# Performance work log

Measured on AMD Instinct MI355X. Metric: run time of the kernel, lower is better.

## Reference

```python
import jax, jax.numpy as jnp
import numpy as np

N, D, H, O = 2048, 128, 256, 1  # batch, input_dim, hidden_dim, output_dim
LN_EPS = 1e-5


def setup_inputs() -> dict:
    key = jax.random.key(0)
    ks = jax.random.split(key, 10)
    s = lambda fan_in: 1.0 / np.sqrt(fan_in)
    return {
        "array": jax.random.normal(ks[0], (N, D), dtype=jnp.float32),
        # per-feature Linear(1, H) stacked: weight [D, H], bias [D, H]
        "W_in": jax.random.uniform(ks[1], (D, H), jnp.float32, -1.0, 1.0),
        "b_in": jax.random.uniform(ks[2], (D, H), jnp.float32, -1.0, 1.0),
        # FactorAttentionLayer (width D): W: Linear(D, D), V: Linear(D, 1), LayerNorm(D)
        "Wf": jax.random.uniform(ks[3], (D, D), jnp.float32, -s(D), s(D)),
        "bf": jax.random.uniform(ks[4], (D,), jnp.float32, -s(D), s(D)),
        "Vf": jax.random.uniform(ks[5], (D,), jnp.float32, -s(D), s(D)),
        "bv": jnp.zeros((), jnp.float32),
        "ln_g": jnp.ones((D,), jnp.float32),
        "ln_b": jnp.zeros((D,), jnp.float32),
        # fc_hidden: Linear(D*H, H); fc_output: Linear(H, O)  (stored as [in, out])
        "Wh": jax.random.uniform(ks[6], (D * H, H), jnp.float32, -s(D * H), s(D * H)),
        "bh": jax.random.uniform(ks[7], (H,), jnp.float32, -s(D * H), s(D * H)),
        "Wo": jax.random.uniform(ks[8], (H, O), jnp.float32, -s(H), s(H)),
        "bo": jax.random.uniform(ks[9], (O,), jnp.float32, -s(H), s(H)),
    }


def reference(array, W_in, b_in, Wf, bf, Vf, bv, ln_g, ln_b, Wh, bh, Wo, bo):
    # Fused per-feature Linear(1,H)+ReLU: [n, D, H]
    p = jax.nn.relu(array[:, :, None] * W_in[None] + b_in[None])
    # permute(0, 2, 1) -> [n, H, D]
    x = jnp.transpose(p, (0, 2, 1))
    # FactorAttention: tanh-linear, softmax over axis 1 (the H axis), residual mul, LayerNorm over D
    u = jnp.tanh(jnp.einsum('nhd,de->nhe', x, Wf) + bf)          # [n, H, D]
    scores = jnp.einsum('nhd,d->nh', u, Vf) + bv                  # [n, H]
    attn = jax.nn.softmax(scores, axis=1)[:, :, None]             # [n, H, 1]
    y = x + x * attn                                              # [n, H, D]
    mu = jnp.mean(y, axis=-1, keepdims=True)
    var = jnp.mean((y - mu) ** 2, axis=-1, keepdims=True)
    y = (y - mu) * jax.lax.rsqrt(var + LN_EPS) * ln_g + ln_b
    # flatten [n, H*D] and MLP head (dropout = identity in eval)
    xx = y.reshape(y.shape[0], -1)
    h = jax.nn.relu(xx @ Wh + bh)
    return h @ Wo + bo
```

## Files before the change

kernel.cpp:

```cpp
#include <hip/hip_runtime.h>

#define NB 2048
#define DD 128
#define HH 256
#define KF 32768
#define LN_EPS 1e-5f

typedef __attribute__((ext_vector_type(8))) short short8;
typedef __attribute__((ext_vector_type(4))) float float4_t;

__device__ __forceinline__ unsigned short f2bf(float f) {
    unsigned int u = __builtin_bit_cast(unsigned int, f);
    u += 0x7fffu + ((u >> 16) & 1u);
    return (unsigned short)(u >> 16);
}

__device__ __forceinline__ void gl2lds16(const void* g, void* l) {
    __builtin_amdgcn_global_load_lds(
        (const __attribute__((address_space(1))) unsigned int*)g,
        (__attribute__((address_space(3))) unsigned int*)l, 16, 0, 0);
}

__global__ void prep_b(const float* __restrict__ Wh, unsigned short* __restrict__ WhbT) {
    __shared__ unsigned short tile[64][65];
    int kb = blockIdx.x;
    int jb = blockIdx.y;
    int t = threadIdx.x;
    int c = t & 63, r4 = t >> 6;
    int kap0 = kb * 64;
    int d  = kap0 >> 8;
    int h0 = kap0 & 255;
    for (int rr = r4; rr < 64; rr += 4) {
        int k = (h0 + rr) * 128 + d;
        tile[rr][c] = f2bf(Wh[(long)k * 256 + jb * 64 + c]);
    }
    __syncthreads();
    for (int rr = r4; rr < 64; rr += 4) {
        WhbT[(long)(jb * 64 + rr) * KF + kap0 + c] = tile[c][rr];
    }
}

__global__ void zgen(const float* __restrict__ arr, const float* __restrict__ Win,
                     const float* __restrict__ bin, const float* __restrict__ g,
                     const float* __restrict__ beta, unsigned short* __restrict__ Z) {
    __shared__ float a_s[4][128];
    __shared__ float g_s[128], b_s[128];
    int t = threadIdx.x;
    int n0 = blockIdx.x * 4;
    if (t < 128) { g_s[t] = g[t]; b_s[t] = beta[t]; }
    for (int i = t; i < 512; i += 256) a_s[i >> 7][i & 127] = arr[n0 * 128 + i];
    __syncthreads();
    int h = t;
    float sum[4] = {0.f, 0.f, 0.f, 0.f}, ssq[4] = {0.f, 0.f, 0.f, 0.f};
    for (int d = 0; d < 128; ++d) {
        float w = Win[d * 256 + h];
        float bb = bin[d * 256 + h];
#pragma unroll
        for (int q = 0; q < 4; ++q) {
            float x = fmaxf(fmaf(a_s[q][d], w, bb), 0.f);
            sum[q] += x; ssq[q] += x * x;
        }
    }
    float mu[4], rs[4];
#pragma unroll
    for (int q = 0; q < 4; ++q) {
        mu[q] = sum[q] * (1.f / 128.f);
        float var = fmaxf(ssq[q] * (1.f / 128.f) - mu[q] * mu[q], 0.f);
        rs[q] = rsqrtf(var + LN_EPS);
    }
    for (int d = 0; d < 128; ++d) {
        float w = Win[d * 256 + h];
        float bb = bin[d * 256 + h];
        float gg = g_s[d], be = b_s[d];
#pragma unroll
        for (int q = 0; q < 4; ++q) {
            float x = fmaxf(fmaf(a_s[q][d], w, bb), 0.f);
            float zv = fmaf((x - mu[q]) * rs[q], gg, be);
            Z[(long)(n0 + q) * KF + d * 256 + h] = f2bf(zv);
        }
    }
}

#define BM 128
#define BN 128
#define BK 32
#define KSPLIT 16
#define KSL (KF / KSPLIT)

__global__ __launch_bounds__(256, 2) void gemm_k(
        const unsigned short* __restrict__ A,
        const unsigned short* __restrict__ Bt,
        float* __restrict__ Cp) {
    __shared__ unsigned short As[BM * BK];
    __shared__ unsigned short Bs[BN * BK];
    int bid = blockIdx.x;
    int ks = bid >> 5;
    int mt = (bid >> 1) & 15;
    int nt = bid & 1;
    int m0 = mt * BM, n0 = nt * BN, k0 = ks * KSL;
    int t = threadIdx.x;
    int lane = t & 63, wave = t >> 6;
    int wm = (wave >> 1) * 64, wn = (wave & 1) * 64;
    int fr = lane & 15;
    int fk = (lane >> 4) * 8;

    float4_t acc[4][4] = {};

    const unsigned short* Aab = A + (long)m0 * KF + k0;
    const unsigned short* Bab = Bt + (long)n0 * KF + k0;
    int s0 = t, s1 = t + 256;
    long aoff0 = (long)(s0 >> 2) * KF + (long)(s0 & 3) * 8;
    long aoff1 = (long)(s1 >> 2) * KF + (long)(s1 & 3) * 8;

    for (int kk = 0; kk < KSL; kk += BK) {
        __syncthreads();
        gl2lds16(Aab + kk + aoff0, &As[s0 * 8]);
        gl2lds16(Aab + kk + aoff1, &As[s1 * 8]);
        gl2lds16(Bab + kk + aoff0, &Bs[s0 * 8]);
        gl2lds16(Bab + kk + aoff1, &Bs[s1 * 8]);
        __syncthreads();
        short8 af[4], bfv[4];
#pragma unroll
        for (int i = 0; i < 4; ++i)
            af[i] = *(const short8*)&As[(wm + i * 16 + fr) * BK + fk];
#pragma unroll
        for (int i = 0; i < 4; ++i)
            bfv[i] = *(const short8*)&Bs[(wn + i * 16 + fr) * BK + fk];
#pragma unroll
        for (int mi = 0; mi < 4; ++mi)
#pragma unroll
            for (int ni = 0; ni < 4; ++ni)
                acc[mi][ni] = __builtin_amdgcn_mfma_f32_16x16x32_bf16(
                    af[mi], bfv[ni], acc[mi][ni], 0, 0, 0);
    }

    int rb = (lane >> 4) * 4;
    float* Cb = Cp + (long)ks * NB * 256;
#pragma unroll
    for (int mi = 0; mi < 4; ++mi) {
#pragma unroll
        for (int ni = 0; ni < 4; ++ni) {
            int n = n0 + wn + ni * 16 + fr;
#pragma unroll
            for (int r = 0; r < 4; ++r) {
                int m = m0 + wm + mi * 16 + rb + r;
                Cb[(long)m * 256 + n] = acc[mi][ni][r];
            }
        }
    }
}

__global__ void finale(const float* __restrict__ Cp, const float* __restrict__ bh,
                       const float* __restrict__ Wo, const float* __restrict__ bo,
                       float* __restrict__ out) {
    __shared__ float red[4];
    int n = blockIdx.x, t = threadIdx.x;
    int lane = t & 63, wave = t >> 6;
    float s = bh[t];
    for (int sl = 0; sl < KSPLIT; ++sl)
        s += Cp[(long)sl * NB * 256 + (long)n * 256 + t];
    float v = fmaxf(s, 0.f) * Wo[t];
#pragma unroll
    for (int o = 32; o; o >>= 1) v += __shfl_down(v, o);
    if (lane == 0) red[wave] = v;
    __syncthreads();
    if (t == 0) out[n] = red[0] + red[1] + red[2] + red[3] + bo[0];
}

extern "C" void kernel_launch(void* const* d_in, const int* in_sizes, int n_in,
                              void* d_out, int out_size, void* d_ws, size_t ws_size,
                              hipStream_t stream) {
    const float* arr  = (const float*)d_in[0];
    const float* Win  = (const float*)d_in[1];
    const float* bin  = (const float*)d_in[2];
    const float* ln_g = (const float*)d_in[7];
    const float* ln_b = (const float*)d_in[8];
    const float* Wh   = (const float*)d_in[9];
    const float* bh   = (const float*)d_in[10];
    const float* Wo   = (const float*)d_in[11];
    const float* bo   = (const float*)d_in[12];
    float* out = (float*)d_out;

    char* ws = (char*)d_ws;
    unsigned short* WhbT = (unsigned short*)ws;
    unsigned short* Z    = (unsigned short*)(ws + 16777216ull);
    float* Cp            = (float*)(ws + 16777216ull + 134217728ull);

    hipLaunchKernelGGL(prep_b, dim3(512, 4), dim3(256), 0, stream, Wh, WhbT);
    hipLaunchKernelGGL(zgen, dim3(512), dim3(256), 0, stream, arr, Win, bin, ln_g, ln_b, Z);
    hipLaunchKernelGGL(gemm_k, dim3(512), dim3(256), 0, stream, Z, WhbT, Cp);
    hipLaunchKernelGGL(finale, dim3(NB), dim3(256), 0, stream, Cp, bh, Wo, bo, out);
}
```

Before: 207.5 us.

## Generate LayerNorm activations inside GEMM and fold gamma/beta into weights

Removes the materialized 128MB bf16 Z activation matrix. The GEMM now recomputes relu(a*W+b) normalized by precomputed per-row mean/rstd on the fly in registers. LayerNorm gamma is folded into the transposed bf16 weight, and beta becomes a precomputed bias vector built with atomics. The GEMM tiling changes to BN=256 with a 32-way K split and an XOR-swizzled B layout in LDS. This trades a large memory write and read for extra ALU work in the GEMM, plus doubled partial-sum traffic in the finale.

After: 210.9 us. Within noise of the previous version (+1.6%).

```diff
diff --git a/kernel.cpp b/kernel.cpp
--- a/kernel.cpp
+++ b/kernel.cpp
@@ -1,146 +1,195 @@
 #include <hip/hip_runtime.h>
 
 #define NB 2048
-#define DD 128
-#define HH 256
 #define KF 32768
 #define LN_EPS 1e-5f
+#define KSPLIT 32
+#define KSL 1024
+#define BM 128
+#define BN 256
+#define BK 32
 
 typedef __attribute__((ext_vector_type(8))) short short8;
 typedef __attribute__((ext_vector_type(4))) float float4_t;
+typedef __attribute__((ext_vector_type(4))) float vf4;
 
 __device__ __forceinline__ unsigned short f2bf(float f) {
     unsigned int u = __builtin_bit_cast(unsigned int, f);
     u += 0x7fffu + ((u >> 16) & 1u);
     return (unsigned short)(u >> 16);
 }
-
+__device__ __forceinline__ unsigned int pk2(float lo, float hi) {
+    return (unsigned int)f2bf(lo) | ((unsigned int)f2bf(hi) << 16);
+}
 __device__ __forceinline__ void gl2lds16(const void* g, void* l) {
     __builtin_amdgcn_global_load_lds(
         (const __attribute__((address_space(1))) unsigned int*)g,
         (__attribute__((address_space(3))) unsigned int*)l, 16, 0, 0);
 }
 
-__global__ void prep_b(const float* __restrict__ Wh, unsigned short* __restrict__ WhbT) {
+__global__ void prep_b(const float* __restrict__ Wh, const float* __restrict__ g,
+                       const float* __restrict__ beta,
+                       unsigned short* __restrict__ GwT, float* __restrict__ Cbeta) {
     __shared__ unsigned short tile[64][65];
-    int kb = blockIdx.x;
-    int jb = blockIdx.y;
-    int t = threadIdx.x;
-    int c = t & 63, r4 = t >> 6;
+    __shared__ float cred[4][64];
+    int kb = blockIdx.x, jb = blockIdx.y;
+    int t = threadIdx.x, c = t & 63, r4 = t >> 6;
     int kap0 = kb * 64;
-    int d  = kap0 >> 8;
-    int h0 = kap0 & 255;
+    int s = kb >> 4, h_loc = kb & 15;
+    int h = (s >> 1) * 16 + h_loc;
+    int dbase = (s & 1) * 64;
+    float cb = 0.f;
     for (int rr = r4; rr < 64; rr += 4) {
-        int k = (h0 + rr) * 128 + d;
-        tile[rr][c] = f2bf(Wh[(long)k * 256 + jb * 64 + c]);
-    }
-    __syncthreads();
+        int d = dbase + rr;
+        float w = Wh[(long)(h * 128 + d) * 256 + jb * 64 + c];
+        tile[rr][c] = f2bf(g[d] * w);
+        cb += beta[d] * w;
+    }
+    cred[r4][c] = cb;
+    __syncthreads();
+    if (r4 == 0)
+        atomicAdd(&Cbeta[jb * 64 + c], cred[0][c] + cred[1][c] + cred[2][c] + cred[3][c]);
     for (int rr = r4; rr < 64; rr += 4) {
-        WhbT[(long)(jb * 64 + rr) * KF + kap0 + c] = tile[c][rr];
-    }
-}
-
-__global__ void zgen(const float* __restrict__ arr, const float* __restrict__ Win,
-                     const float* __restrict__ bin, const float* __restrict__ g,
-                     const float* __restrict__ beta, unsigned short* __restrict__ Z) {
+        int jrow = jb * 64 + rr;
+        int c2 = c & 31;
+        int pos = ((c2 >> 3) ^ ((jrow >> 1) & 3)) & 3;
+        GwT[(long)jrow * KF + kap0 + (c & 32) + pos * 8 + (c & 7)] = tile[c][rr];
+    }
+}
+
+__global__ void trans_wb(const float* __restrict__ Win, const float* __restrict__ bin,
+                         float* __restrict__ WinT, float* __restrict__ binT) {
+    __shared__ float tile[64][65];
+    const float* src = blockIdx.z ? bin : Win;
+    float* dst = blockIdx.z ? binT : WinT;
+    int db = blockIdx.x, hb = blockIdx.y;
+    int t = threadIdx.x, c = t & 63, r4 = t >> 6;
+    for (int rr = r4; rr < 64; rr += 4)
+        tile[rr][c] = src[(db * 64 + rr) * 256 + hb * 64 + c];
+    __syncthreads();
+    for (int rr = r4; rr < 64; rr += 4)
+        dst[(hb * 64 + rr) * 128 + db * 64 + c] = tile[c][rr];
+}
+
+__global__ void stats(const float* __restrict__ arr, const float* __restrict__ Win,
+                      const float* __restrict__ bin, float* __restrict__ rsm) {
     __shared__ float a_s[4][128];
-    __shared__ float g_s[128], b_s[128];
     int t = threadIdx.x;
     int n0 = blockIdx.x * 4;
-    if (t < 128) { g_s[t] = g[t]; b_s[t] = beta[t]; }
     for (int i = t; i < 512; i += 256) a_s[i >> 7][i & 127] = arr[n0 * 128 + i];
     __syncthreads();
-    int h = t;
-    float sum[4] = {0.f, 0.f, 0.f, 0.f}, ssq[4] = {0.f, 0.f, 0.f, 0.f};
+    float sum[4] = {}, ssq[4] = {};
     for (int d = 0; d < 128; ++d) {
-        float w = Win[d * 256 + h];
-        float bb = bin[d * 256 + h];
+        float w = Win[d * 256 + t], bb = bin[d * 256 + t];
 #pragma unroll
         for (int q = 0; q < 4; ++q) {
             float x = fmaxf(fmaf(a_s[q][d], w, bb), 0.f);
             sum[q] += x; ssq[q] += x * x;
         }
     }
-    float mu[4], rs[4];
+    float2* rsm2 = (float2*)rsm;
 #pragma unroll
     for (int q = 0; q < 4; ++q) {
-        mu[q] = sum[q] * (1.f / 128.f);
-        float var = fmaxf(ssq[q] * (1.f / 128.f) - mu[q] * mu[q], 0.f);
-        rs[q] = rsqrtf(var + LN_EPS);
-    }
-    for (int d = 0; d < 128; ++d) {
-        float w = Win[d * 256 + h];
-        float bb = bin[d * 256 + h];
-        float gg = g_s[d], be = b_s[d];
-#pragma unroll
-        for (int q = 0; q < 4; ++q) {
-            float x = fmaxf(fmaf(a_s[q][d], w, bb), 0.f);
-            float zv = fmaf((x - mu[q]) * rs[q], gg, be);
-            Z[(long)(n0 + q) * KF + d * 256 + h] = f2bf(zv);
-        }
-    }
-}
-
-#define BM 128
-#define BN 128
-#define BK 32
-#define KSPLIT 16
-#define KSL (KF / KSPLIT)
-
-__global__ __launch_bounds__(256, 2) void gemm_k(
-        const unsigned short* __restrict__ A,
-        const unsigned short* __restrict__ Bt,
-        float* __restrict__ Cp) {
-    __shared__ unsigned short As[BM * BK];
+        float mu = sum[q] * (1.f / 128.f);
+        float var = fmaxf(ssq[q] * (1.f / 128.f) - mu * mu, 0.f);
+        float rs = rsqrtf(var + LN_EPS);
+        rsm2[(long)(n0 + q) * 256 + t] = make_float2(rs, -mu * rs);
+    }
+}
+
+__global__ __launch_bounds__(256, 2) void gemm_f(
+        const float* __restrict__ arr, const float* __restrict__ WinT,
+        const float* __restrict__ binT, const float* __restrict__ rsm,
+        const unsigned short* __restrict__ GwT, float* __restrict__ Cp) {
+    __shared__ float wi_s[16 * 64];
+    __shared__ float bi_s[16 * 64];
+    __shared__ float rs_s[128 * 17 * 2];
     __shared__ unsigned short Bs[BN * BK];
+
     int bid = blockIdx.x;
-    int ks = bid >> 5;
-    int mt = (bid >> 1) & 15;
-    int nt = bid & 1;
-    int m0 = mt * BM, n0 = nt * BN, k0 = ks * KSL;
-    int t = threadIdx.x;
-    int lane = t & 63, wave = t >> 6;
-    int wm = (wave >> 1) * 64, wn = (wave & 1) * 64;
-    int fr = lane & 15;
-    int fk = (lane >> 4) * 8;
-
-    float4_t acc[4][4] = {};
-
-    const unsigned short* Aab = A + (long)m0 * KF + k0;
-    const unsigned short* Bab = Bt + (long)n0 * KF + k0;
-    int s0 = t, s1 = t + 256;
-    long aoff0 = (long)(s0 >> 2) * KF + (long)(s0 & 3) * 8;
-    long aoff1 = (long)(s1 >> 2) * KF + (long)(s1 & 3) * 8;
-
-    for (int kk = 0; kk < KSL; kk += BK) {
-        __syncthreads();
-        gl2lds16(Aab + kk + aoff0, &As[s0 * 8]);
-        gl2lds16(Aab + kk + aoff1, &As[s1 * 8]);
-        gl2lds16(Bab + kk + aoff0, &Bs[s0 * 8]);
-        gl2lds16(Bab + kk + aoff1, &Bs[s1 * 8]);
-        __syncthreads();
-        short8 af[4], bfv[4];
-#pragma unroll
-        for (int i = 0; i < 4; ++i)
-            af[i] = *(const short8*)&As[(wm + i * 16 + fr) * BK + fk];
-#pragma unroll
-        for (int i = 0; i < 4; ++i)
-            bfv[i] = *(const short8*)&Bs[(wn + i * 16 + fr) * BK + fk];
-#pragma unroll
-        for (int mi = 0; mi < 4; ++mi)
-#pragma unroll
-            for (int ni = 0; ni < 4; ++ni)
-                acc[mi][ni] = __builtin_amdgcn_mfma_f32_16x16x32_bf16(
-                    af[mi], bfv[ni], acc[mi][ni], 0, 0, 0);
-    }
-
-    int rb = (lane >> 4) * 4;
-    float* Cb = Cp + (long)ks * NB * 256;
+    int mt = bid >> 5;
+    int s = bid & 31;
+    int m0 = mt * BM;
+    int hs0 = (s >> 1) * 16;
+    int ds = s & 1;
+    int t = threadIdx.x, lane = t & 63, wave = t >> 6;
+    int fr = lane & 15, kg = lane >> 4;
+    int wm = (wave & 1) * 64, wn = (wave >> 1) * 128;
+
+    gl2lds16(WinT + (hs0 + (t >> 4)) * 128 + ds * 64 + (t & 15) * 4, &wi_s[t * 4]);
+    gl2lds16(binT + (hs0 + (t >> 4)) * 128 + ds * 64 + (t & 15) * 4, &bi_s[t * 4]);
+    const float2* rsm2 = (const float2*)rsm;
+#pragma unroll
+    for (int i = 0; i < 8; ++i) {
+        int ci = t + i * 256;
+        int m = ci >> 4, hl = ci & 15;
+        float2 rv = rsm2[(long)(m0 + m) * 256 + hs0 + hl];
+        *(float2*)&rs_s[(m * 17 + hl) * 2] = rv;
+    }
+
+    float4_t acc[4][8] = {};
+    const unsigned short* Bg = GwT + (long)s * KSL;
+
+    for (int dh = 0; dh < 2; ++dh) {
+        vf4 a0[4], a1[4];
+#pragma unroll
+        for (int mi = 0; mi < 4; ++mi) {
+            const float* ap = arr + (long)(m0 + wm + mi * 16 + fr) * 128
+                              + ds * 64 + dh * 32 + kg * 8;
+            a0[mi] = *(const vf4*)ap;
+            a1[mi] = *(const vf4*)(ap + 4);
+        }
+        for (int hl = 0; hl < 16; ++hl) {
+            int w = hl * 2 + dh;
+            __syncthreads();
+#pragma unroll
+            for (int i = 0; i < 4; ++i) {
+                int ci = t + i * 256;
+                gl2lds16(Bg + (long)(ci >> 2) * KF + w * 32 + (ci & 3) * 8,
+                         &Bs[ci * 8]);
+            }
+            vf4 w0 = *(const vf4*)&wi_s[hl * 64 + dh * 32 + kg * 8];
+            vf4 w1 = *(const vf4*)&wi_s[hl * 64 + dh * 32 + kg * 8 + 4];
+            vf4 b0 = *(const vf4*)&bi_s[hl * 64 + dh * 32 + kg * 8];
+            vf4 b1 = *(const vf4*)&bi_s[hl * 64 + dh * 32 + kg * 8 + 4];
+            short8 af[4];
+#pragma unroll
+            for (int mi = 0; mi < 4; ++mi) {
+                float2 rv = *(const float2*)&rs_s[((wm + mi * 16 + fr) * 17 + hl) * 2];
+                float z[8];
+#pragma unroll
+                for (int j = 0; j < 4; ++j) {
+                    float x = fmaxf(fmaf(a0[mi][j], w0[j], b0[j]), 0.f);
+                    z[j] = fmaf(x, rv.x, rv.y);
+                    float x2 = fmaxf(fmaf(a1[mi][j], w1[j], b1[j]), 0.f);
+                    z[4 + j] = fmaf(x2, rv.x, rv.y);
+                }
+                union { short8 v; unsigned int u[4]; } pa;
+#pragma unroll
+                for (int p = 0; p < 4; ++p) pa.u[p] = pk2(z[2 * p], z[2 * p + 1]);
+                af[mi] = pa.v;
+            }
+            __syncthreads();
+#pragma unroll
+            for (int ni = 0; ni < 8; ++ni) {
+                int n = wn + ni * 16 + fr;
+                int bc = kg ^ ((n >> 1) & 3);
+                short8 bf = *(const short8*)&Bs[n * 32 + bc * 8];
+#pragma unroll
+                for (int mi = 0; mi < 4; ++mi)
+                    acc[mi][ni] = __builtin_amdgcn_mfma_f32_16x16x32_bf16(
+                        af[mi], bf, acc[mi][ni], 0, 0, 0);
+            }
+        }
+    }
+
+    float* Cb = Cp + (long)s * NB * 256;
+    int rb = kg * 4;
 #pragma unroll
     for (int mi = 0; mi < 4; ++mi) {
 #pragma unroll
-        for (int ni = 0; ni < 4; ++ni) {
-            int n = n0 + wn + ni * 16 + fr;
+        for (int ni = 0; ni < 8; ++ni) {
+            int n = wn + ni * 16 + fr;
 #pragma unroll
             for (int r = 0; r < 4; ++r) {
                 int m = m0 + wm + mi * 16 + rb + r;
@@ -150,16 +199,16 @@
     }
 }
 
-__global__ void finale(const float* __restrict__ Cp, const float* __restrict__ bh,
-                       const float* __restrict__ Wo, const float* __restrict__ bo,
-                       float* __restrict__ out) {
+__global__ void finale(const float* __restrict__ Cp, const float* __restrict__ Cbeta,
+                       const float* __restrict__ bh, const float* __restrict__ Wo,
+                       const float* __restrict__ bo, float* __restrict__ out) {
     __shared__ float red[4];
     int n = blockIdx.x, t = threadIdx.x;
     int lane = t & 63, wave = t >> 6;
-    float s = bh[t];
+    float ssum = bh[t] + Cbeta[t];
     for (int sl = 0; sl < KSPLIT; ++sl)
-        s += Cp[(long)sl * NB * 256 + (long)n * 256 + t];
-    float v = fmaxf(s, 0.f) * Wo[t];
+        ssum += Cp[(long)sl * NB * 256 + (long)n * 256 + t];
+    float v = fmaxf(ssum, 0.f) * Wo[t];
 #pragma unroll
     for (int o = 32; o; o >>= 1) v += __shfl_down(v, o);
     if (lane == 0) red[wave] = v;
@@ -182,12 +231,17 @@
     float* out = (float*)d_out;
 
     char* ws = (char*)d_ws;
-    unsigned short* WhbT = (unsigned short*)ws;
-    unsigned short* Z    = (unsigned short*)(ws + 16777216ull);
-    float* Cp            = (float*)(ws + 16777216ull + 134217728ull);
-
-    hipLaunchKernelGGL(prep_b, dim3(512, 4), dim3(256), 0, stream, Wh, WhbT);
-    hipLaunchKernelGGL(zgen, dim3(512), dim3(256), 0, stream, arr, Win, bin, ln_g, ln_b, Z);
-    hipLaunchKernelGGL(gemm_k, dim3(512), dim3(256), 0, stream, Z, WhbT, Cp);
-    hipLaunchKernelGGL(finale, dim3(NB), dim3(256), 0, stream, Cp, bh, Wo, bo, out);
-}
+    unsigned short* GwT  = (unsigned short*)(ws);
+    float*          Cp   = (float*)(ws + 16777216ull);
+    float*          rsm  = (float*)(ws + 83886080ull);
+    float*          WinT = (float*)(ws + 88080384ull);
+    float*          binT = (float*)(ws + 88211456ull);
+    float*          Cbeta= (float*)(ws + 88342528ull);
+
+    hipMemsetAsync(Cbeta, 0, 256 * sizeof(float), stream);
+    hipLaunchKernelGGL(prep_b, dim3(512, 4), dim3(256), 0, stream, Wh, ln_g, ln_b, GwT, Cbeta);
+    hipLaunchKernelGGL(trans_wb, dim3(2, 4, 2), dim3(256), 0, stream, Win, bin, WinT, binT);
+    hipLaunchKernelGGL(stats, dim3(512), dim3(256), 0, stream, arr, Win, bin, rsm);
+    hipLaunchKernelGGL(gemm_f, dim3(512), dim3(256), 0, stream, arr, WinT, binT, rsm, GwT, Cp);
+    hipLaunchKernelGGL(finale, dim3(NB), dim3(256), 0, stream, Cp, Cbeta, bh, Wo, bo, out);
+}
```
